# Optimization experiments

Hardware: AMD Instinct MI355X
Metric: run time of the kernel (lower is better)

Reference implementation:

```python
import jax, jax.numpy as jnp
import numpy as np

EPS = 1e-07  # DIoULoss eps


def setup_inputs() -> dict:
    key = jax.random.key(0)
    k1, k2, k3, k4, k5 = jax.random.split(key, 5)
    B, Q = 32, 131072
    # valid xyxy boxes: uniform centers in [0,100), sizes in [1,51)
    def make_boxes(kc, ks):
        c = jax.random.uniform(kc, (B, Q, 2), dtype=jnp.float32) * 100.0
        wh = jax.random.uniform(ks, (B, Q, 2), dtype=jnp.float32) * 50.0 + 1.0
        return jnp.concatenate([c - wh / 2, c + wh / 2], axis=-1)
    inputs = make_boxes(k1, k2)
    targets = make_boxes(k3, k4)
    mask = jax.random.randint(k5, (B, Q), 0, 2).astype(jnp.bool_)
    num_boxes = 2097152
    return {"inputs": inputs, "targets": targets, "mask": mask, "num_boxes": num_boxes}


def _diou_loss(b1, b2):
    # b1, b2: (N, 4) xyxy. Per-pair GIoU == diagonal of the original NxN matrix.
    a1 = (b1[:, 2] - b1[:, 0]) * (b1[:, 3] - b1[:, 1])
    a2 = (b2[:, 2] - b2[:, 0]) * (b2[:, 3] - b2[:, 1])
    lt = jnp.maximum(b1[:, :2], b2[:, :2])
    rb = jnp.minimum(b1[:, 2:], b2[:, 2:])
    wh = jnp.clip(rb - lt, 0.0)
    inter = wh[:, 0] * wh[:, 1]
    union = a1 + a2 - inter
    iou = inter / union
    lt_c = jnp.minimum(b1[:, :2], b2[:, :2])
    rb_c = jnp.maximum(b1[:, 2:], b2[:, 2:])
    wh_c = rb_c - lt_c  # boxes are valid so enclose extent >= 0
    area_c = wh_c[:, 0] * wh_c[:, 1]
    giou = iou - (area_c - union) / area_c
    # DIoU penalty: squared center distance / squared enclosing diagonal
    c1 = (b1[:, :2] + b1[:, 2:]) * 0.5
    c2 = (b2[:, :2] + b2[:, 2:]) * 0.5
    d2 = jnp.sum((c1 - c2) ** 2, axis=1)
    diag2 = wh_c[:, 0] ** 2 + wh_c[:, 1] ** 2
    diou = giou - d2 / (diag2 + EPS)
    return 1.0 - diou


def reference(inputs, targets, mask, num_boxes):
    B, Q, _ = inputs.shape
    loss = _diou_loss(inputs.reshape(-1, 4), targets.reshape(-1, 4)).reshape(B, Q)
    loss = loss * mask.astype(loss.dtype)
    # reduction='mean' with num_boxes provided -> sum / num_boxes
    return loss.sum() / num_boxes
```

## Files before the change

### kernel.cpp

```cpp
#include <hip/hip_runtime.h>

#define DIOU_EPS 1e-7f

__global__ void zero_out_kernel(float* out) {
    out[0] = 0.0f;
}

__global__ __launch_bounds__(256) void diou_loss_kernel(
    const float4* __restrict__ boxes1,
    const float4* __restrict__ boxes2,
    const int* __restrict__ mask,
    const int* __restrict__ num_boxes,
    float* __restrict__ out,
    int n)
{
    int tid = blockIdx.x * blockDim.x + threadIdx.x;
    int stride = gridDim.x * blockDim.x;

    float acc = 0.0f;
    for (int i = tid; i < n; i += stride) {
        float4 a = boxes1[i];
        float4 b = boxes2[i];
        float m = (float)(mask[i] != 0);

        float a1 = (a.z - a.x) * (a.w - a.y);
        float a2 = (b.z - b.x) * (b.w - b.y);

        float ltx = fmaxf(a.x, b.x);
        float lty = fmaxf(a.y, b.y);
        float rbx = fminf(a.z, b.z);
        float rby = fminf(a.w, b.w);
        float iw = fmaxf(rbx - ltx, 0.0f);
        float ih = fmaxf(rby - lty, 0.0f);
        float inter = iw * ih;
        float uni = a1 + a2 - inter;
        float iou = inter / uni;

        float ex0 = fminf(a.x, b.x);
        float ey0 = fminf(a.y, b.y);
        float ex1 = fmaxf(a.z, b.z);
        float ey1 = fmaxf(a.w, b.w);
        float wc = ex1 - ex0;
        float hc = ey1 - ey0;
        float area_c = wc * hc;

        float giou = iou - (area_c - uni) / area_c;

        float c1x = (a.x + a.z) * 0.5f;
        float c1y = (a.y + a.w) * 0.5f;
        float c2x = (b.x + b.z) * 0.5f;
        float c2y = (b.y + b.w) * 0.5f;
        float dx = c1x - c2x;
        float dy = c1y - c2y;
        float d2 = dx * dx + dy * dy;
        float diag2 = wc * wc + hc * hc;

        float diou = giou - d2 / (diag2 + DIOU_EPS);
        acc += m * (1.0f - diou);
    }

    #pragma unroll
    for (int off = 32; off > 0; off >>= 1)
        acc += __shfl_down(acc, off, 64);

    __shared__ float wave_sums[4];
    int wave = threadIdx.x >> 6;
    if ((threadIdx.x & 63) == 0) wave_sums[wave] = acc;
    __syncthreads();

    if (threadIdx.x == 0) {
        float s = wave_sums[0] + wave_sums[1] + wave_sums[2] + wave_sums[3];
        float inv_nb = 1.0f / (float)num_boxes[0];
        atomicAdd(out, s * inv_nb);
    }
}

extern "C" void kernel_launch(void* const* d_in, const int* in_sizes, int n_in,
                              void* d_out, int out_size, void* d_ws, size_t ws_size,
                              hipStream_t stream) {
    const float4* boxes1 = (const float4*)d_in[0];
    const float4* boxes2 = (const float4*)d_in[1];
    const int* mask = (const int*)d_in[2];
    const int* num_boxes = (const int*)d_in[3];

    float* out = (float*)d_out;
    int n = in_sizes[2];

    zero_out_kernel<<<1, 1, 0, stream>>>(out);

    const int block = 256;
    const int grid = 2048;
    diou_loss_kernel<<<grid, block, 0, stream>>>(boxes1, boxes2, mask, num_boxes, out, n);
}
```

Baseline: 174.4 us.

## Replace grid-stride loop with one-chunk-per-block batched loads

Each block now processes a fixed chunk of 1024 boxes, with every thread loading four box pairs and masks up front before computing. This raises memory-level parallelism compared to the old grid-stride loop that issued one load set per iteration. The grid scales with n, which doubles the number of blocks and the number of atomicAdds to the single output, adding some contention. The DIoU math is factored into a helper with minor algebraic simplification of the center distance.

```diff
diff --git a/kernel.cpp b/kernel.cpp
--- a/kernel.cpp
+++ b/kernel.cpp
@@ -1,12 +1,42 @@
 #include <hip/hip_runtime.h>
 
 #define DIOU_EPS 1e-7f
+
+constexpr int BLOCK = 256;
+constexpr int ITEMS = 4;
+constexpr int CHUNK = BLOCK * ITEMS;
 
 __global__ void zero_out_kernel(float* out) {
     out[0] = 0.0f;
 }
 
-__global__ __launch_bounds__(256) void diou_loss_kernel(
+__device__ __forceinline__ float diou_elem(float4 a, float4 b, int m) {
+    float a1 = (a.z - a.x) * (a.w - a.y);
+    float a2 = (b.z - b.x) * (b.w - b.y);
+
+    float iw = fmaxf(fminf(a.z, b.z) - fmaxf(a.x, b.x), 0.0f);
+    float ih = fmaxf(fminf(a.w, b.w) - fmaxf(a.y, b.y), 0.0f);
+    float inter = iw * ih;
+    float uni = a1 + a2 - inter;
+    float iou = inter / uni;
+
+    float wc = fmaxf(a.z, b.z) - fminf(a.x, b.x);
+    float hc = fmaxf(a.w, b.w) - fminf(a.y, b.y);
+    float area_c = wc * hc;
+
+    float giou = iou - (area_c - uni) / area_c;
+
+    float dx = (a.x + a.z - b.x - b.z) * 0.5f;
+    float dy = (a.y + a.w - b.y - b.w) * 0.5f;
+    float d2 = dx * dx + dy * dy;
+    float diag2 = wc * wc + hc * hc;
+
+    float diou = giou - d2 / (diag2 + DIOU_EPS);
+    float mf = (float)(m != 0);
+    return mf * (1.0f - diou);
+}
+
+__global__ __launch_bounds__(BLOCK) void diou_loss_kernel(
     const float4* __restrict__ boxes1,
     const float4* __restrict__ boxes2,
     const int* __restrict__ mask,
@@ -14,61 +44,41 @@
     float* __restrict__ out,
     int n)
 {
-    int tid = blockIdx.x * blockDim.x + threadIdx.x;
-    int stride = gridDim.x * blockDim.x;
+    const int t = threadIdx.x;
+    const int base = blockIdx.x * CHUNK;
 
     float acc = 0.0f;
-    for (int i = tid; i < n; i += stride) {
-        float4 a = boxes1[i];
-        float4 b = boxes2[i];
-        float m = (float)(mask[i] != 0);
 
-        float a1 = (a.z - a.x) * (a.w - a.y);
-        float a2 = (b.z - b.x) * (b.w - b.y);
+    if (base + CHUNK <= n) {
+        float4 A[ITEMS], B[ITEMS];
+        int    M[ITEMS];
+        #pragma unroll
+        for (int j = 0; j < ITEMS; ++j) A[j] = boxes1[base + j * BLOCK + t];
+        #pragma unroll
+        for (int j = 0; j < ITEMS; ++j) B[j] = boxes2[base + j * BLOCK + t];
+        #pragma unroll
+        for (int j = 0; j < ITEMS; ++j) M[j] = mask[base + j * BLOCK + t];
 
-        float ltx = fmaxf(a.x, b.x);
-        float lty = fmaxf(a.y, b.y);
-        float rbx = fminf(a.z, b.z);
-        float rby = fminf(a.w, b.w);
-        float iw = fmaxf(rbx - ltx, 0.0f);
-        float ih = fmaxf(rby - lty, 0.0f);
-        float inter = iw * ih;
-        float uni = a1 + a2 - inter;
-        float iou = inter / uni;
-
-        float ex0 = fminf(a.x, b.x);
-        float ey0 = fminf(a.y, b.y);
-        float ex1 = fmaxf(a.z, b.z);
-        float ey1 = fmaxf(a.w, b.w);
-        float wc = ex1 - ex0;
-        float hc = ey1 - ey0;
-        float area_c = wc * hc;
-
-        float giou = iou - (area_c - uni) / area_c;
-
-        float c1x = (a.x + a.z) * 0.5f;
-        float c1y = (a.y + a.w) * 0.5f;
-        float c2x = (b.x + b.z) * 0.5f;
-        float c2y = (b.y + b.w) * 0.5f;
-        float dx = c1x - c2x;
-        float dy = c1y - c2y;
-        float d2 = dx * dx + dy * dy;
-        float diag2 = wc * wc + hc * hc;
-
-        float diou = giou - d2 / (diag2 + DIOU_EPS);
-        acc += m * (1.0f - diou);
+        #pragma unroll
+        for (int j = 0; j < ITEMS; ++j) acc += diou_elem(A[j], B[j], M[j]);
+    } else {
+        #pragma unroll
+        for (int j = 0; j < ITEMS; ++j) {
+            int i = base + j * BLOCK + t;
+            if (i < n) acc += diou_elem(boxes1[i], boxes2[i], mask[i]);
+        }
     }
 
     #pragma unroll
     for (int off = 32; off > 0; off >>= 1)
         acc += __shfl_down(acc, off, 64);
 
-    __shared__ float wave_sums[4];
-    int wave = threadIdx.x >> 6;
-    if ((threadIdx.x & 63) == 0) wave_sums[wave] = acc;
+    __shared__ float wave_sums[BLOCK / 64];
+    int wave = t >> 6;
+    if ((t & 63) == 0) wave_sums[wave] = acc;
     __syncthreads();
 
-    if (threadIdx.x == 0) {
+    if (t == 0) {
         float s = wave_sums[0] + wave_sums[1] + wave_sums[2] + wave_sums[3];
         float inv_nb = 1.0f / (float)num_boxes[0];
         atomicAdd(out, s * inv_nb);
@@ -88,7 +98,6 @@
 
     zero_out_kernel<<<1, 1, 0, stream>>>(out);
 
-    const int block = 256;
-    const int grid = 2048;
-    diou_loss_kernel<<<grid, block, 0, stream>>>(boxes1, boxes2, mask, num_boxes, out, n);
+    int grid = (n + CHUNK - 1) / CHUNK;
+    diou_loss_kernel<<<grid, BLOCK, 0, stream>>>(boxes1, boxes2, mask, num_boxes, out, n);
 }
```

Result: slower. 178.9 us (+2.6%).
